# Kernel optimization log

Hardware: AMD Instinct MI355X
Metric: run time of the kernel (lower is better)

The kernel has to match this reference:

```python
import jax, jax.numpy as jnp
import numpy as np

# Config mirrors init_kwargs
B = 8            # batch_size
L = 1024         # new tokens per sequence (prefill)
BS = 16          # block_size
MAXB = 128       # max_blocks_per_seq = ceil(2048/16)
H = 8            # num_kv_heads
D = 128          # head_dim
NLAYERS = 2
TOTAL = B * MAXB * NLAYERS  # 2048 total blocks


def setup_inputs() -> dict:
    key = jax.random.key(0)
    k1, k2 = jax.random.split(key)
    return {
        "layer_idx": 0,
        "key_states": jax.random.normal(k1, (B * L, H, D), jnp.float32),
        "value_states": jax.random.normal(k2, (B * L, H, D), jnp.float32),
        "input_len": jnp.full((B,), L, jnp.int32),
        "cu_seqlens": (jnp.arange(B + 1, dtype=jnp.int32) * L),
        "k_cache": jnp.zeros((TOTAL, H, BS, D), jnp.float32),
        "v_cache": jnp.zeros((TOTAL, H, BS, D), jnp.float32),
        "block_tables": jnp.zeros((B, MAXB), jnp.int32),  # layer slice
        "seq_lens": jnp.zeros((B,), jnp.int32),           # layer slice
        "free_blocks": jnp.arange(TOTAL, dtype=jnp.int32),
    }


def reference(layer_idx, key_states, value_states, input_len, cu_seqlens,
              k_cache, v_cache, block_tables, seq_lens, free_blocks):
    # ---- block allocation (vectorized form of the per-sequence python loop) ----
    old_nb = (seq_lens + BS - 1) // BS                 # blocks already held
    new_nb = (seq_lens + input_len + BS - 1) // BS     # blocks needed
    alloc = new_nb - old_nb                            # per-seq new blocks
    cum = jnp.cumsum(alloc)                            # tail-pop order: seq i gets
    num_free = free_blocks.shape[0]                    # free_blocks[num_free-cum[i] : ...]
    start = num_free - cum                             # [B]
    slots = jnp.arange(MAXB, dtype=jnp.int32)[None, :]                  # [1, MAXB]
    valid = (slots >= old_nb[:, None]) & (slots < new_nb[:, None])      # [B, MAXB]
    free_idx = jnp.clip(start[:, None] + (slots - old_nb[:, None]), 0, num_free - 1)
    bt = jnp.where(valid, free_blocks[free_idx], block_tables)          # updated table

    # ---- scatter new K/V tokens into paged cache (store_paged_kv) ----
    # assumes uniform input_len == L (as built in setup_inputs)
    t = jnp.arange(L, dtype=jnp.int32)[None, :]        # [1, L]
    tok_idx = cu_seqlens[:B][:, None] + t              # [B, L] index into packed K/V
    pos = seq_lens[:, None] + t                        # absolute position in sequence
    blk = jnp.take_along_axis(bt, pos // BS, axis=1)   # [B, L] physical block id
    off = pos % BS                                     # [B, L] offset within block

    keys = key_states[tok_idx.ravel()]                 # [B*L, H, D]
    vals = value_states[tok_idx.ravel()]
    k_new = k_cache.at[blk.ravel(), :, off.ravel(), :].set(keys)
    v_new = v_cache.at[blk.ravel(), :, off.ravel(), :].set(vals)
    return jnp.stack([k_new, v_new])  # [2, TOTAL, H, BS, D]
```

## Files before the change

### kernel.cpp

```cpp
#include <hip/hip_runtime.h>

constexpr int B     = 8;
constexpr int L     = 1024;
constexpr int BS    = 16;
constexpr int MAXB  = 128;
constexpr int H     = 8;
constexpr int D     = 128;
constexpr int TOTAL = 2048;
constexpr int CACHE_ELEMS = TOTAL * H * BS * D;

__global__ void build_inv_kernel(const int* __restrict__ input_len,
                                 const int* __restrict__ block_tables,
                                 const int* __restrict__ seq_lens,
                                 const int* __restrict__ free_blocks,
                                 int* __restrict__ inv) {
    const int tid = threadIdx.x;
    for (int i = tid; i < TOTAL; i += blockDim.x) inv[i] = -1;
    __syncthreads();

    int old_nb[B], new_nb[B], start[B];
    int cum = 0;
    for (int b = 0; b < B; ++b) {
        const int sl = seq_lens[b];
        old_nb[b] = (sl + BS - 1) / BS;
        new_nb[b] = (sl + input_len[b] + BS - 1) / BS;
        cum += new_nb[b] - old_nb[b];
        start[b] = TOTAL - cum;
    }

    for (int b = 0; b < B; ++b) {
        const int j0 = seq_lens[b] / BS;
        for (int j = j0 + tid; j < new_nb[b]; j += blockDim.x) {
            int blk;
            if (j >= old_nb[b]) {
                int fi = start[b] + (j - old_nb[b]);
                fi = min(max(fi, 0), TOTAL - 1);
                blk = free_blocks[fi];
            } else {
                blk = block_tables[b * MAXB + j];
            }
            inv[blk] = (b << 20) | j;
        }
    }
}

__global__ __launch_bounds__(256) void gather_out_kernel(
        const float4* __restrict__ key_states,
        const float4* __restrict__ value_states,
        const float4* __restrict__ k_cache,
        const float4* __restrict__ v_cache,
        const int*    __restrict__ input_len,
        const int*    __restrict__ cu_seqlens,
        const int*    __restrict__ seq_lens,
        const int*    __restrict__ inv,
        float4*       __restrict__ out) {
    constexpr int C4   = CACHE_ELEMS / 4;
    constexpr int PB4  = H * BS * D / 4;
    constexpr int PH4  = BS * D / 4;
    constexpr int PO4  = D / 4;

    const int idx4 = blockIdx.x * blockDim.x + threadIdx.x;
    if (idx4 >= 2 * C4) return;

    const int c    = idx4 >= C4 ? 1 : 0;
    const int rel4 = idx4 - c * C4;

    const int blk = rel4 / PB4;
    int r         = rel4 - blk * PB4;
    const int h   = r / PH4;  r -= h * PH4;
    const int off = r / PO4;
    const int d4  = r - off * PO4;

    const int m = inv[blk];
    float4 val;
    bool from_cache = true;
    if (m >= 0) {
        const int b   = m >> 20;
        const int j   = m & 0xFFFFF;
        const int pos = j * BS + off;
        const int sl  = seq_lens[b];
        if (pos >= sl && pos < sl + input_len[b]) {
            const int tok = cu_seqlens[b] + (pos - sl);
            const float4* __restrict__ src = c ? value_states : key_states;
            val = src[tok * (H * D / 4) + h * PO4 + d4];
            from_cache = false;
        }
    }
    if (from_cache) {
        const float4* __restrict__ cache = c ? v_cache : k_cache;
        val = cache[rel4];
    }
    out[idx4] = val;
}

extern "C" void kernel_launch(void* const* d_in, const int* in_sizes, int n_in,
                              void* d_out, int out_size, void* d_ws, size_t ws_size,
                              hipStream_t stream) {
    const float* key_states   = (const float*)d_in[1];
    const float* value_states = (const float*)d_in[2];
    const int*   input_len    = (const int*)d_in[3];
    const int*   cu_seqlens   = (const int*)d_in[4];
    const float* k_cache      = (const float*)d_in[5];
    const float* v_cache      = (const float*)d_in[6];
    const int*   block_tables = (const int*)d_in[7];
    const int*   seq_lens     = (const int*)d_in[8];
    const int*   free_blocks  = (const int*)d_in[9];

    int* inv = (int*)d_ws;

    build_inv_kernel<<<1, 256, 0, stream>>>(input_len, block_tables, seq_lens,
                                            free_blocks, inv);

    const int total4 = 2 * CACHE_ELEMS / 4;
    const int blocks = (total4 + 255) / 256;
    gather_out_kernel<<<blocks, 256, 0, stream>>>(
        (const float4*)key_states, (const float4*)value_states,
        (const float4*)k_cache, (const float4*)v_cache,
        input_len, cu_seqlens, seq_lens, inv, (float4*)d_out);
}
```

Measured before the change: 473.7 us.

## Fuse block-inverse build into per-block gather kernel with nontemporal copies

Drops the separate single-block inverse-table kernel. Each of the 2048 workgroups now scans the allocation tables itself to find which sequence slot maps to its physical block, then copies K and V for that block with nontemporal loads and stores. This removes a serialized tiny launch, the workspace round trip and the per-element index math. In exchange every workgroup redundantly scans up to about 1024 table entries, and the copy loop gives each thread 16 float4 elements instead of one.

```diff
diff --git a/kernel.cpp b/kernel.cpp
--- a/kernel.cpp
+++ b/kernel.cpp
@@ -1,96 +1,100 @@
 #include <hip/hip_runtime.h>
 
+typedef float float4n __attribute__((ext_vector_type(4)));
+
 constexpr int B     = 8;
-constexpr int L     = 1024;
 constexpr int BS    = 16;
 constexpr int MAXB  = 128;
 constexpr int H     = 8;
 constexpr int D     = 128;
 constexpr int TOTAL = 2048;
-constexpr int CACHE_ELEMS = TOTAL * H * BS * D;
 
-__global__ void build_inv_kernel(const int* __restrict__ input_len,
-                                 const int* __restrict__ block_tables,
-                                 const int* __restrict__ seq_lens,
-                                 const int* __restrict__ free_blocks,
-                                 int* __restrict__ inv) {
-    const int tid = threadIdx.x;
-    for (int i = tid; i < TOTAL; i += blockDim.x) inv[i] = -1;
+constexpr int C4   = TOTAL * H * BS * D / 4;
+constexpr int PB4  = H * BS * D / 4;
+constexpr int PT4  = H * D / 4;
+constexpr int PO4  = D / 4;
+
+__global__ __launch_bounds__(256) void paged_kv_kernel(
+        const float4n* __restrict__ key_states,
+        const float4n* __restrict__ value_states,
+        const float4n* __restrict__ k_cache,
+        const float4n* __restrict__ v_cache,
+        const int*     __restrict__ input_len,
+        const int*     __restrict__ cu_seqlens,
+        const int*     __restrict__ block_tables,
+        const int*     __restrict__ seq_lens,
+        const int*     __restrict__ free_blocks,
+        float4n*       __restrict__ out) {
+    const int myblk = blockIdx.x;
+    const int tid   = threadIdx.x;
+
+    __shared__ int s_found;
+    if (tid == 0) s_found = -1;
     __syncthreads();
 
-    int old_nb[B], new_nb[B], start[B];
     int cum = 0;
+    #pragma unroll
     for (int b = 0; b < B; ++b) {
-        const int sl = seq_lens[b];
-        old_nb[b] = (sl + BS - 1) / BS;
-        new_nb[b] = (sl + input_len[b] + BS - 1) / BS;
-        cum += new_nb[b] - old_nb[b];
-        start[b] = TOTAL - cum;
-    }
-
-    for (int b = 0; b < B; ++b) {
-        const int j0 = seq_lens[b] / BS;
-        for (int j = j0 + tid; j < new_nb[b]; j += blockDim.x) {
-            int blk;
-            if (j >= old_nb[b]) {
-                int fi = start[b] + (j - old_nb[b]);
+        const int sl  = seq_lens[b];
+        const int il  = input_len[b];
+        const int onb = (sl + BS - 1) >> 4;
+        const int nnb = (sl + il + BS - 1) >> 4;
+        cum += nnb - onb;
+        const int st  = TOTAL - cum;
+        const int j0  = sl >> 4;
+        for (int j = j0 + tid; j < nnb; j += 256) {
+            int cand;
+            if (j >= onb) {
+                int fi = st + (j - onb);
                 fi = min(max(fi, 0), TOTAL - 1);
-                blk = free_blocks[fi];
+                cand = free_blocks[fi];
             } else {
-                blk = block_tables[b * MAXB + j];
+                cand = block_tables[b * MAXB + j];
             }
-            inv[blk] = (b << 20) | j;
+            if (cand == myblk) s_found = (b << 20) | j;
         }
     }
-}
+    __syncthreads();
+    const int m = s_found;
 
-__global__ __launch_bounds__(256) void gather_out_kernel(
-        const float4* __restrict__ key_states,
-        const float4* __restrict__ value_states,
-        const float4* __restrict__ k_cache,
-        const float4* __restrict__ v_cache,
-        const int*    __restrict__ input_len,
-        const int*    __restrict__ cu_seqlens,
-        const int*    __restrict__ seq_lens,
-        const int*    __restrict__ inv,
-        float4*       __restrict__ out) {
-    constexpr int C4   = CACHE_ELEMS / 4;
-    constexpr int PB4  = H * BS * D / 4;
-    constexpr int PH4  = BS * D / 4;
-    constexpr int PO4  = D / 4;
+    const int base4 = myblk * PB4;
 
-    const int idx4 = blockIdx.x * blockDim.x + threadIdx.x;
-    if (idx4 >= 2 * C4) return;
-
-    const int c    = idx4 >= C4 ? 1 : 0;
-    const int rel4 = idx4 - c * C4;
-
-    const int blk = rel4 / PB4;
-    int r         = rel4 - blk * PB4;
-    const int h   = r / PH4;  r -= h * PH4;
-    const int off = r / PO4;
-    const int d4  = r - off * PO4;
-
-    const int m = inv[blk];
-    float4 val;
-    bool from_cache = true;
-    if (m >= 0) {
-        const int b   = m >> 20;
-        const int j   = m & 0xFFFFF;
-        const int pos = j * BS + off;
-        const int sl  = seq_lens[b];
-        if (pos >= sl && pos < sl + input_len[b]) {
-            const int tok = cu_seqlens[b] + (pos - sl);
-            const float4* __restrict__ src = c ? value_states : key_states;
-            val = src[tok * (H * D / 4) + h * PO4 + d4];
-            from_cache = false;
+    if (m < 0) {
+        #pragma unroll 4
+        for (int t = 0; t < PB4 / 256; ++t) {
+            const int i4 = (t << 8) + tid;
+            float4n k = __builtin_nontemporal_load(&k_cache[base4 + i4]);
+            float4n v = __builtin_nontemporal_load(&v_cache[base4 + i4]);
+            __builtin_nontemporal_store(k, &out[base4 + i4]);
+            __builtin_nontemporal_store(v, &out[C4 + base4 + i4]);
+        }
+    } else {
+        const int b  = m >> 20;
+        const int j  = m & 0xFFFFF;
+        const int sl = seq_lens[b];
+        const int il = input_len[b];
+        const int cu = cu_seqlens[b];
+        #pragma unroll 4
+        for (int t = 0; t < PB4 / 256; ++t) {
+            const int i4  = (t << 8) + tid;
+            const int h   = i4 >> 9;
+            const int off = (i4 >> 5) & 15;
+            const int d4  = i4 & 31;
+            const int pos = j * BS + off;
+            float4n k, v;
+            if (pos >= sl && pos < sl + il) {
+                const int tok = cu + (pos - sl);
+                const int si  = tok * PT4 + h * PO4 + d4;
+                k = __builtin_nontemporal_load(&key_states[si]);
+                v = __builtin_nontemporal_load(&value_states[si]);
+            } else {
+                k = __builtin_nontemporal_load(&k_cache[base4 + i4]);
+                v = __builtin_nontemporal_load(&v_cache[base4 + i4]);
+            }
+            __builtin_nontemporal_store(k, &out[base4 + i4]);
+            __builtin_nontemporal_store(v, &out[C4 + base4 + i4]);
         }
     }
-    if (from_cache) {
-        const float4* __restrict__ cache = c ? v_cache : k_cache;
-        val = cache[rel4];
-    }
-    out[idx4] = val;
 }
 
 extern "C" void kernel_launch(void* const* d_in, const int* in_sizes, int n_in,
@@ -106,15 +110,9 @@
     const int*   seq_lens     = (const int*)d_in[8];
     const int*   free_blocks  = (const int*)d_in[9];
 
-    int* inv = (int*)d_ws;
-
-    build_inv_kernel<<<1, 256, 0, stream>>>(input_len, block_tables, seq_lens,
-                                            free_blocks, inv);
-
-    const int total4 = 2 * CACHE_ELEMS / 4;
-    const int blocks = (total4 + 255) / 256;
-    gather_out_kernel<<<blocks, 256, 0, stream>>>(
-        (const float4*)key_states, (const float4*)value_states,
-        (const float4*)k_cache, (const float4*)v_cache,
-        input_len, cu_seqlens, seq_lens, inv, (float4*)d_out);
+    paged_kv_kernel<<<TOTAL, 256, 0, stream>>>(
+        (const float4n*)key_states, (const float4n*)value_states,
+        (const float4n*)k_cache, (const float4n*)v_cache,
+        input_len, cu_seqlens, block_tables, seq_lens, free_blocks,
+        (float4n*)d_out);
 }
```

Measured after the change: 475.9 us, median of 2. About the same (+0.5%).
